# Kernel tuning notes

Hardware: AMD Instinct MI355X
Metric: run time of the kernel (lower is better)

## Reference

```python
import jax, jax.numpy as jnp
import numpy as np
from jax.ops import segment_sum, segment_max, segment_min

N_NODES = 200000
N_HE = 100000     # number of hyperedges (nets)
NNZ = 1000000     # number of pins (node,hyperedge) incidences
F_RAW = 29        # raw node features; +2 fake_pos +1 ismacro = 32 = num_features
PIN_D = 4
C = 64            # nhid (heads = 1)
N_MACRO = 512
NUM_CLASSES = 1
SLOPE = 0.1


def _lrelu(v):
    return jnp.where(v >= 0, v, SLOPE * v)


def setup_inputs() -> dict:
    key = jax.random.key(0)
    ks = jax.random.split(key, 16)
    x = jax.random.normal(ks[0], (N_NODES, F_RAW), jnp.float32)
    fake_pos = jax.random.uniform(ks[1], (N_NODES, 2), dtype=jnp.float32)
    node_idx = jax.random.randint(ks[2], (NNZ,), 0, N_NODES)
    he_idx = jax.random.randint(ks[3], (NNZ,), 0, N_HE)
    edge_index = jnp.stack([node_idx, he_idx]).astype(jnp.int32)
    pin_feature = jax.random.normal(ks[4], (NNZ, PIN_D), jnp.float32)
    macro_index = jax.random.randint(ks[5], (N_MACRO,), 0, N_NODES).astype(jnp.int32)
    F_IN = F_RAW + 3

    def lin(k, fi, fo):
        return (jax.random.normal(k, (fi, fo), jnp.float32) / np.float32(np.sqrt(fi)))

    W1 = lin(ks[6], F_IN, C); b1 = jnp.zeros((C,), jnp.float32)
    Wpin = lin(ks[7], PIN_D, C)
    att = jax.random.normal(ks[8], (2 * C,), jnp.float32) / np.float32(np.sqrt(2 * C))
    Wpost = lin(ks[9], 4 * C, C); bpost = jnp.zeros((C,), jnp.float32)
    Wm1 = lin(ks[10], 2 * C, C); bm1 = jnp.zeros((C,), jnp.float32)
    Wm2 = lin(ks[11], C, C // 2); bm2 = jnp.zeros((C // 2,), jnp.float32)
    Wm3 = lin(ks[12], C // 2, NUM_CLASSES); bm3 = jnp.zeros((NUM_CLASSES,), jnp.float32)
    return dict(x=x, fake_pos=fake_pos, edge_index=edge_index, pin_feature=pin_feature,
                macro_index=macro_index, W1=W1, b1=b1, Wpin=Wpin, att=att,
                Wpost=Wpost, bpost=bpost, Wm1=Wm1, bm1=bm1, Wm2=Wm2, bm2=bm2,
                Wm3=Wm3, bm3=bm3)


def _forward(x, fake_pos, edge_index, pin_feature, macro_index,
             W1, b1, Wpin, att, Wpost, bpost, Wm1, bm1, Wm2, bm2, Wm3, bm3):
    node_idx = edge_index[0]
    he_idx = edge_index[1]

    ismacro = jnp.zeros((N_NODES, 1), x.dtype).at[macro_index].set(1.0)
    h = jnp.concatenate([x, fake_pos, ismacro], axis=-1)  # (N, 32)

    xl = h @ W1 + b1                                      # (N, C) node embedding
    pin_m = pin_feature @ Wpin                            # (NNZ, C) pin embedding

    # node -> hyperedge aggregation (mean over incident pins)
    msg_ne = xl[node_idx] + pin_m                         # (NNZ, C)
    deg_e = segment_sum(jnp.ones((NNZ,), x.dtype), he_idx, num_segments=N_HE)
    e_feat = segment_sum(msg_ne, he_idx, num_segments=N_HE) / jnp.maximum(deg_e, 1.0)[:, None]

    # attention over incident hyperedges, softmax per node
    e_g = e_feat[he_idx]                                  # (NNZ, C)
    a_raw = _lrelu(jnp.concatenate([xl[node_idx], e_g], axis=-1) @ att)  # (NNZ,)
    m = segment_max(a_raw, node_idx, num_segments=N_NODES)
    m = jnp.where(jnp.isfinite(m), m, 0.0)
    ex = jnp.exp(a_raw - m[node_idx])
    den = segment_sum(ex, node_idx, num_segments=N_NODES)
    alpha = ex / (den[node_idx] + 1e-16)

    # hyperedge -> node: PNA multi-aggregation of attention-weighted messages
    msg = e_g * alpha[:, None]                            # (NNZ, C)
    deg_n = segment_sum(jnp.ones((NNZ,), x.dtype), node_idx, num_segments=N_NODES)
    deg_c = jnp.maximum(deg_n, 1.0)[:, None]
    s = segment_sum(msg, node_idx, num_segments=N_NODES)
    mean = s / deg_c
    mx = segment_max(msg, node_idx, num_segments=N_NODES)
    mx = jnp.where(deg_n[:, None] > 0, mx, 0.0)
    mn = segment_min(msg, node_idx, num_segments=N_NODES)
    mn = jnp.where(deg_n[:, None] > 0, mn, 0.0)
    sq = segment_sum(msg * msg, node_idx, num_segments=N_NODES) / deg_c
    std = jnp.sqrt(jnp.maximum(sq - mean * mean, 0.0) + 1e-12)

    pna = jnp.concatenate([mean, mx, mn, std], axis=-1) @ Wpost + bpost  # (N, C)
    hx = _lrelu(pna)

    # masked global-mean pools (single graph: batch is all zeros)
    pooled = jnp.concatenate([hx[macro_index].mean(0), hx.mean(0)])[None, :]  # (1, 2C)

    z = _lrelu(pooled @ Wm1 + bm1)
    z = _lrelu(z @ Wm2 + bm2)
    return z @ Wm3 + bm3                                  # (1, num_classes)


def reference(x, fake_pos, edge_index, pin_feature, macro_index,
              W1, b1, Wpin, att, Wpost, bpost, Wm1, bm1, Wm2, bm2, Wm3, bm3):
    return _forward(x, fake_pos, edge_index, pin_feature, macro_index,
                    W1, b1, Wpin, att, Wpost, bpost, Wm1, bm1, Wm2, bm2, Wm3, bm3)
```

## Files before the change

### kernel.cpp

```cpp
#include <hip/hip_runtime.h>
#include <math.h>

#define N_NODES 200000
#define N_HE    100000
#define NNZ     1000000
#define F_RAW   29
#define N_MACRO 512
#define SLOPE   0.1f
#define L_TOTAL (N_NODES + N_HE)
#define NB_SCAN 293

typedef __attribute__((ext_vector_type(8))) short bf16x8;
typedef __attribute__((ext_vector_type(4))) float f32x4;

__device__ __forceinline__ float lrelu(float v) { return v >= 0.f ? v : SLOPE * v; }
__device__ __forceinline__ float bf2f(unsigned short u) { return __uint_as_float(((unsigned)u) << 16); }
__device__ __forceinline__ unsigned short f2bf(float f) {
    unsigned u = __float_as_uint(f);
    unsigned r = u + 0x7FFFu + ((u >> 16) & 1u);
    return (unsigned short)(r >> 16);
}
__device__ __forceinline__ float bflo(unsigned u) { return __uint_as_float(u << 16); }
__device__ __forceinline__ float bfhi(unsigned u) { return __uint_as_float(u & 0xffff0000u); }

__global__ __launch_bounds__(256) void fill_f32(float* p, long long n, float v) {
    long long i = (long long)blockIdx.x * blockDim.x + threadIdx.x;
    long long st = (long long)gridDim.x * blockDim.x;
    for (; i < n; i += st) p[i] = v;
}

__global__ __launch_bounds__(256) void k_pre(
    const int* __restrict__ mi, float* __restrict__ ismacro, int* __restrict__ mcount,
    const float* __restrict__ W1, const float* __restrict__ b1,
    const float* __restrict__ att, float* __restrict__ va,
    const int* __restrict__ nidx, const int* __restrict__ hidx,
    int* __restrict__ cnt, int* __restrict__ rank_n, int* __restrict__ rank_e)
{
    if (blockIdx.x == 0) {
        int t = threadIdx.x;
        if (t < 32) {
            float a = 0.f;
            for (int c = 0; c < 64; c++) a += W1[t * 64 + c] * att[c];
            va[t] = a;
        } else if (t == 32) {
            float a = 0.f;
            for (int c = 0; c < 64; c++) a += b1[c] * att[c];
            va[32] = a;
        }
    } else if (blockIdx.x <= 2) {
        int i = (blockIdx.x - 1) * 256 + threadIdx.x;
        if (i < N_MACRO) {
            ismacro[mi[i]] = 1.0f;
            atomicAdd(&mcount[mi[i]], 1);
        }
    } else {
        int i = (blockIdx.x - 3) * 256 + threadIdx.x;
        int st = (gridDim.x - 3) * 256;
        for (int p = i; p < NNZ; p += st) {
            rank_n[p] = atomicAdd(&cnt[nidx[p]], 1);
            rank_e[p] = atomicAdd(&cnt[N_NODES + hidx[p]], 1);
        }
    }
}

__global__ __launch_bounds__(256) void k_scan1(const int* __restrict__ cnt,
                                               int* __restrict__ row_ptr, int* __restrict__ partials)
{
    __shared__ int sA[256], sB[256];
    const int t = threadIdx.x;
    const int base = blockIdx.x * 1024 + t * 4;
    int v0 = base + 0 < L_TOTAL ? cnt[base + 0] : 0;
    int v1 = base + 1 < L_TOTAL ? cnt[base + 1] : 0;
    int v2 = base + 2 < L_TOTAL ? cnt[base + 2] : 0;
    int v3 = base + 3 < L_TOTAL ? cnt[base + 3] : 0;
    sA[t] = v0 + v1 + v2 + v3;
    __syncthreads();
    int* src = sA; int* dst = sB;
    for (int off = 1; off < 256; off <<= 1) {
        int v = src[t];
        if (t >= off) v += src[t - off];
        dst[t] = v;
        __syncthreads();
        int* tmp = src; src = dst; dst = tmp;
    }
    int excl = t > 0 ? src[t - 1] : 0;
    if (base + 0 < L_TOTAL) row_ptr[base + 0] = excl;
    if (base + 1 < L_TOTAL) row_ptr[base + 1] = excl + v0;
    if (base + 2 < L_TOTAL) row_ptr[base + 2] = excl + v0 + v1;
    if (base + 3 < L_TOTAL) row_ptr[base + 3] = excl + v0 + v1 + v2;
    if (t == 255) partials[blockIdx.x] = src[255];
}

__global__ __launch_bounds__(512) void k_scan2(int* __restrict__ partials)
{
    __shared__ int sA[512], sB[512];
    const int t = threadIdx.x;
    sA[t] = t < NB_SCAN ? partials[t] : 0;
    __syncthreads();
    int* src = sA; int* dst = sB;
    for (int off = 1; off < 512; off <<= 1) {
        int v = src[t];
        if (t >= off) v += src[t - off];
        dst[t] = v;
        __syncthreads();
        int* tmp = src; src = dst; dst = tmp;
    }
    if (t < NB_SCAN) partials[t] = t > 0 ? src[t - 1] : 0;
    if (t == 0) partials[NB_SCAN] = src[511];
}

__global__ __launch_bounds__(256) void k_scan3(int* __restrict__ row_ptr, const int* __restrict__ partials)
{
    const int base = blockIdx.x * 1024 + threadIdx.x * 4;
    int add = partials[blockIdx.x];
    #pragma unroll
    for (int k = 0; k < 4; k++)
        if (base + k < L_TOTAL) row_ptr[base + k] += add;
    if (blockIdx.x == 0 && threadIdx.x == 0) row_ptr[L_TOTAL] = partials[NB_SCAN];
}

__global__ __launch_bounds__(256) void k_mid(
    const int* __restrict__ nidx, const int* __restrict__ hidx,
    const int* __restrict__ row_ptr,
    const int* __restrict__ rank_n, const int* __restrict__ rank_e,
    const float4* __restrict__ pf4, int* __restrict__ csr_n, int4* __restrict__ rec,
    const float* __restrict__ x, const float* __restrict__ fp,
    const float* __restrict__ ismacro, const float* __restrict__ va,
    unsigned short* __restrict__ h, float* __restrict__ xn_att)
{
    if (blockIdx.x < 2048) {
        int i = blockIdx.x * 256 + threadIdx.x;
        int st = 2048 * 256;
        for (int p = i; p < NNZ; p += st) {
            int n = nidx[p], e = hidx[p];
            csr_n[row_ptr[n] + rank_n[p]] = e;
            int pe = row_ptr[N_NODES + e] + rank_e[p];
            float4 q = pf4[p];
            int4 r;
            r.x = n;
            r.y = (int)((unsigned)f2bf(q.x) | ((unsigned)f2bf(q.y) << 16));
            r.z = (int)((unsigned)f2bf(q.z) | ((unsigned)f2bf(q.w) << 16));
            r.w = 0;
            rec[pe - NNZ] = r;
        }
    } else {
        const int lane = threadIdx.x & 63;
        const int half = lane >> 5, k = lane & 31;
        int wid = ((blockIdx.x - 2048) * 256 + threadIdx.x) >> 6;
        int nw = (1024 * 256) >> 6;
        float vak = va[k];
        float c0 = va[32];
        for (int base = wid * 2; base < N_NODES; base += nw * 2) {
            int n = base + half;
            float v;
            if (k < 29)       v = x[(size_t)n * F_RAW + k];
            else if (k == 29) v = fp[2 * n];
            else if (k == 30) v = fp[2 * n + 1];
            else              v = ismacro[n];
            h[(size_t)n * 32 + k] = f2bf(v);
            float r = v * vak;
            #pragma unroll
            for (int o = 16; o > 0; o >>= 1) r += __shfl_xor(r, o, 32);
            if (k == 0) xn_att[n] = r + c0;
        }
    }
}

__global__ __launch_bounds__(256) void k_he_agg(
    const int* __restrict__ row_ptr, const int4* __restrict__ rec,
    const float* __restrict__ W1, const float* __restrict__ Wpin,
    const float* __restrict__ b1, const float* __restrict__ att,
    const unsigned short* __restrict__ h,
    unsigned short* __restrict__ e_feat, float* __restrict__ e_att)
{
    __shared__ float sW1[32 * 64];
    __shared__ float sWp[4 * 64];
    __shared__ float sb1[64];
    for (int i = threadIdx.x; i < 32 * 64; i += 256) sW1[i] = W1[i];
    for (int i = threadIdx.x; i < 4 * 64; i += 256) sWp[i] = Wpin[i];
    if (threadIdx.x < 64) sb1[threadIdx.x] = b1[threadIdx.x];
    __syncthreads();
    const int lane = threadIdx.x & 63;
    const int g  = lane >> 3;
    const int gl = lane & 7;
    float att2 = att[64 + lane];
    int wid = (blockIdx.x * blockDim.x + threadIdx.x) >> 6;
    int nw = (gridDim.x * blockDim.x) >> 6;
    for (int e = wid; e < N_HE; e += nw) {
        int start = row_ptr[N_NODES + e];
        int deg = row_ptr[N_NODES + e + 1] - start;
        float h0 = 0.f, h1 = 0.f, h2 = 0.f, h3 = 0.f;
        float pa = 0.f, pb = 0.f;
        const int4* rbase = rec + (start - NNZ);
        int t = g;
        for (; t + 8 < deg; t += 16) {
            int4 rA = rbase[t];
            int4 rB = rbase[t + 8];
            ushort4 uA = *(const ushort4*)&h[(size_t)rA.x * 32 + 4 * gl];
            ushort4 uB = *(const ushort4*)&h[(size_t)rB.x * 32 + 4 * gl];
            h0 += bf2f(uA.x) + bf2f(uB.x);
            h1 += bf2f(uA.y) + bf2f(uB.y);
            h2 += bf2f(uA.z) + bf2f(uB.z);
            h3 += bf2f(uA.w) + bf2f(uB.w);
            unsigned pyA = (gl == 0) ? (unsigned)rA.y : ((gl == 1) ? (unsigned)rA.z : 0u);
            unsigned pyB = (gl == 0) ? (unsigned)rB.y : ((gl == 1) ? (unsigned)rB.z : 0u);
            pa += bflo(pyA) + bflo(pyB);
            pb += bfhi(pyA) + bfhi(pyB);
        }
        if (t < deg) {
            int4 r = rbase[t];
            ushort4 u = *(const ushort4*)&h[(size_t)r.x * 32 + 4 * gl];
            h0 += bf2f(u.x); h1 += bf2f(u.y); h2 += bf2f(u.z); h3 += bf2f(u.w);
            unsigned py = (gl == 0) ? (unsigned)r.y : ((gl == 1) ? (unsigned)r.z : 0u);
            pa += bflo(py); pb += bfhi(py);
        }
        #pragma unroll
        for (int o = 8; o <= 32; o <<= 1) {
            h0 += __shfl_xor(h0, o); h1 += __shfl_xor(h1, o);
            h2 += __shfl_xor(h2, o); h3 += __shfl_xor(h3, o);
            pa += __shfl_xor(pa, o); pb += __shfl_xor(pb, o);
        }
        float p0 = __shfl(pa, 0, 64), p1 = __shfl(pb, 0, 64);
        float p2 = __shfl(pa, 1, 64), p3 = __shfl(pb, 1, 64);
        float acc = (float)deg * sb1[lane]
                  + p0 * sWp[lane] + p1 * sWp[64 + lane]
                  + p2 * sWp[128 + lane] + p3 * sWp[192 + lane];
        #pragma unroll
        for (int kk = 0; kk < 8; kk++) {
            float a0 = __shfl(h0, kk, 64), a1 = __shfl(h1, kk, 64);
            float a2 = __shfl(h2, kk, 64), a3 = __shfl(h3, kk, 64);
            acc += a0 * sW1[(4 * kk + 0) * 64 + lane] + a1 * sW1[(4 * kk + 1) * 64 + lane]
                 + a2 * sW1[(4 * kk + 2) * 64 + lane] + a3 * sW1[(4 * kk + 3) * 64 + lane];
        }
        float d = (float)(deg > 0 ? deg : 1);
        float v = acc / d;
        e_feat[(size_t)e * 64 + lane] = f2bf(v);
        float r = v * att2;
        #pragma unroll
        for (int o = 32; o > 0; o >>= 1) r += __shfl_down(r, o, 64);
        if (lane == 0) e_att[e] = r;
    }
}

__global__ __launch_bounds__(256, 4) void k_fused(
    const int* __restrict__ row_ptr, const int* __restrict__ csr,
    const float* __restrict__ xn_att, const float* __restrict__ e_att,
    const unsigned short* __restrict__ e_feat,
    const float* __restrict__ Wpost, const float* __restrict__ bpost,
    const int* __restrict__ mcount,
    float* __restrict__ sum_all, float* __restrict__ sum_mac)
{
    __shared__ __align__(16) unsigned short scat[16 * 264];
    const int lane = threadIdx.x & 63;
    const int wave = threadIdx.x >> 6;
    const int half = lane >> 5;
    const int c2   = lane & 31;
    const int quad = lane >> 4;
    const int nn   = lane & 15;
    bf16x8 wfrag[8];
    #pragma unroll
    for (int s = 0; s < 8; s++) {
        bf16x8 w;
        #pragma unroll
        for (int j = 0; j < 8; j++)
            w[j] = (short)f2bf(Wpost[(size_t)(32 * s + quad * 8 + j) * 64 + wave * 16 + nn]);
        wfrag[s] = w;
    }
    float bias = bpost[wave * 16 + nn];
    float pool = 0.f, pmac = 0.f;
    const int nbatches = N_NODES / 16;
    for (int b = blockIdx.x; b < nbatches; b += gridDim.x) {
        const int base = b * 16;
        __syncthreads();
        for (int i = 0; i < 4; i++) {
            int j = wave * 4 + i;
            int n = base + j;
            int start = row_ptr[n];
            int deg = row_ptr[n + 1] - start;
            float xn = xn_att[n];
            float sw = 0.f;
            float sx = 0.f, sy = 0.f, qx = 0.f, qy = 0.f;
            float mxx = -INFINITY, mxy = -INFINITY, mnx = INFINITY, mny = INFINITY;
            int t = half;
            for (; t + 2 < deg; t += 4) {
                int e0 = csr[start + t];
                int e1 = csr[start + t + 2];
                float w0 = __expf(lrelu(xn + e_att[e0]));
                float w1 = __expf(lrelu(xn + e_att[e1]));
                unsigned u0 = ((const unsigned*)&e_feat[(size_t)e0 * 64])[c2];
                unsigned u1 = ((const unsigned*)&e_feat[(size_t)e1 * 64])[c2];
                float v0x = bflo(u0) * w0, v0y = bfhi(u0) * w0;
                float v1x = bflo(u1) * w1, v1y = bfhi(u1) * w1;
                sw += w0 + w1;
                sx += v0x + v1x; sy += v0y + v1y;
                qx += v0x * v0x + v1x * v1x; qy += v0y * v0y + v1y * v1y;
                mxx = fmaxf(mxx, fmaxf(v0x, v1x)); mxy = fmaxf(mxy, fmaxf(v0y, v1y));
                mnx = fminf(mnx, fminf(v0x, v1x)); mny = fminf(mny, fminf(v0y, v1y));
            }
            for (; t < deg; t += 2) {
                int e = csr[start + t];
                float w = __expf(lrelu(xn + e_att[e]));
                unsigned u = ((const unsigned*)&e_feat[(size_t)e * 64])[c2];
                float vx = bflo(u) * w, vy = bfhi(u) * w;
                sw += w; sx += vx; sy += vy; qx += vx * vx; qy += vy * vy;
                mxx = fmaxf(mxx, vx); mxy = fmaxf(mxy, vy);
                mnx = fminf(mnx, vx); mny = fminf(mny, vy);
            }
            sw  += __shfl_xor(sw, 32);
            sx  += __shfl_xor(sx, 32);  sy += __shfl_xor(sy, 32);
            qx  += __shfl_xor(qx, 32);  qy += __shfl_xor(qy, 32);
            mxx = fmaxf(mxx, __shfl_xor(mxx, 32)); mxy = fmaxf(mxy, __shfl_xor(mxy, 32));
            mnx = fminf(mnx, __shfl_xor(mnx, 32)); mny = fminf(mny, __shfl_xor(mny, 32));
            float invD = 1.f / (sw + 1e-16f);
            float dc = (float)(deg > 0 ? deg : 1);
            float meanx = sx * invD / dc, meany = sy * invD / dc;
            float sqmx = qx * invD * invD / dc, sqmy = qy * invD * invD / dc;
            float stdx = sqrtf(fmaxf(sqmx - meanx * meanx, 0.f) + 1e-12f);
            float stdy = sqrtf(fmaxf(sqmy - meany * meany, 0.f) + 1e-12f);
            ushort2* row = (ushort2*)&scat[j * 264];
            if (half == 0) {
                ushort2 a; a.x = f2bf(meanx); a.y = f2bf(meany);
                row[c2] = a;
                ushort2 bmax; bmax.x = f2bf(deg > 0 ? mxx * invD : 0.f);
                bmax.y = f2bf(deg > 0 ? mxy * invD : 0.f);
                row[32 + c2] = bmax;
            } else {
                ushort2 bmin; bmin.x = f2bf(deg > 0 ? mnx * invD : 0.f);
                bmin.y = f2bf(deg > 0 ? mny * invD : 0.f);
                row[64 + c2] = bmin;
                ushort2 bstd; bstd.x = f2bf(stdx); bstd.y = f2bf(stdy);
                row[96 + c2] = bstd;
            }
        }
        __syncthreads();
        f32x4 acc = {0.f, 0.f, 0.f, 0.f};
        #pragma unroll
        for (int s = 0; s < 8; s++) {
            bf16x8 a = *(const bf16x8*)&scat[nn * 264 + 32 * s + quad * 8];
            acc = __builtin_amdgcn_mfma_f32_16x16x32_bf16(a, wfrag[s], acc, 0, 0, 0);
        }
        int4 mc4 = *(const int4*)&mcount[base + 4 * quad];
        float h0 = lrelu(acc[0] + bias);
        float h1 = lrelu(acc[1] + bias);
        float h2 = lrelu(acc[2] + bias);
        float h3 = lrelu(acc[3] + bias);
        pool += h0 + h1 + h2 + h3;
        pmac += (float)mc4.x * h0 + (float)mc4.y * h1 + (float)mc4.z * h2 + (float)mc4.w * h3;
    }
    pool += __shfl_xor(pool, 16); pool += __shfl_xor(pool, 32);
    pmac += __shfl_xor(pmac, 16); pmac += __shfl_xor(pmac, 32);
    if (quad == 0) {
        atomicAdd(&sum_all[wave * 16 + nn], pool);
        atomicAdd(&sum_mac[wave * 16 + nn], pmac);
    }
}

__global__ __launch_bounds__(256) void k_final(
    const float* __restrict__ sum_all, const float* __restrict__ sum_mac,
    const float* __restrict__ Wm1, const float* __restrict__ bm1,
    const float* __restrict__ Wm2, const float* __restrict__ bm2,
    const float* __restrict__ Wm3, const float* __restrict__ bm3,
    float* __restrict__ out)
{
    __shared__ float spool[128];
    __shared__ float z1[64];
    __shared__ float z2[32];
    if (threadIdx.x < 64) {
        spool[threadIdx.x]      = sum_mac[threadIdx.x] / (float)N_MACRO;
        spool[64 + threadIdx.x] = sum_all[threadIdx.x] / (float)N_NODES;
    }
    __syncthreads();
    if (threadIdx.x < 64) {
        int j = threadIdx.x;
        float a = bm1[j];
        #pragma unroll 4
        for (int k = 0; k < 128; k++) a += spool[k] * Wm1[k * 64 + j];
        z1[j] = lrelu(a);
    }
    __syncthreads();
    if (threadIdx.x < 32) {
        int j = threadIdx.x;
        float a = bm2[j];
        #pragma unroll 4
        for (int k = 0; k < 64; k++) a += z1[k] * Wm2[k * 32 + j];
        z2[j] = lrelu(a);
    }
    __syncthreads();
    if (threadIdx.x == 0) {
        float a = bm3[0];
        #pragma unroll
        for (int k = 0; k < 32; k++) a += z2[k] * Wm3[k];
        out[0] = a;
    }
}

extern "C" void kernel_launch(void* const* d_in, const int* in_sizes, int n_in,
                              void* d_out, int out_size, void* d_ws, size_t ws_size,
                              hipStream_t stream)
{
    const float* x        = (const float*)d_in[0];
    const float* fake_pos = (const float*)d_in[1];
    const int*   edge     = (const int*)d_in[2];
    const float* pinf     = (const float*)d_in[3];
    const int*   macro    = (const int*)d_in[4];
    const float* W1    = (const float*)d_in[5];
    const float* b1    = (const float*)d_in[6];
    const float* Wpin  = (const float*)d_in[7];
    const float* att   = (const float*)d_in[8];
    const float* Wpost = (const float*)d_in[9];
    const float* bpost = (const float*)d_in[10];
    const float* Wm1   = (const float*)d_in[11];
    const float* bm1   = (const float*)d_in[12];
    const float* Wm2   = (const float*)d_in[13];
    const float* bm2   = (const float*)d_in[14];
    const float* Wm3   = (const float*)d_in[15];
    const float* bm3   = (const float*)d_in[16];
    float* out = (float*)d_out;

    float* ws = (float*)d_ws;
    float*    ismacro = ws;
    float*    sum_all = ws + 200000;
    float*    sum_mac = ws + 200064;
    int*      mcount  = (int*)(ws + 200128);
    int*      cnt     = (int*)(ws + 400128);
    int*      row_ptr  = (int*)(ws + 700128);
    int*      partials = (int*)(ws + 1000132);
    float*    va       = ws + 1000432;
    int*      rank_n   = (int*)(ws + 1000472);
    int*      rank_e   = (int*)(ws + 2000472);
    int*      csr_n    = (int*)(ws + 3000472);
    int4*     rec      = (int4*)(ws + 4000472);
    float*    e_att    = ws + 8000472;
    float*    xn_att   = ws + 8100472;
    unsigned short* h      = (unsigned short*)(ws + 8300472);
    unsigned short* e_feat = (unsigned short*)(ws + 11500472);

    const int* nidx = edge;
    const int* hidx = edge + NNZ;

    fill_f32<<<1024, 256, 0, stream>>>(ws, 700128LL, 0.f);
    k_pre<<<2051, 256, 0, stream>>>(macro, ismacro, mcount, W1, b1, att, va,
                                    nidx, hidx, cnt, rank_n, rank_e);
    k_scan1<<<NB_SCAN, 256, 0, stream>>>(cnt, row_ptr, partials);
    k_scan2<<<1, 512, 0, stream>>>(partials);
    k_scan3<<<NB_SCAN, 256, 0, stream>>>(row_ptr, partials);
    k_mid<<<3072, 256, 0, stream>>>(nidx, hidx, row_ptr, rank_n, rank_e,
                                    (const float4*)pinf, csr_n, rec,
                                    x, fake_pos, ismacro, va, h, xn_att);
    k_he_agg<<<2048, 256, 0, stream>>>(row_ptr, rec, W1, Wpin, b1, att, h, e_feat, e_att);
    k_fused<<<2048, 256, 0, stream>>>(row_ptr, csr_n, xn_att, e_att, e_feat, Wpost, bpost,
                                      mcount, sum_all, sum_mac);
    k_final<<<1, 256, 0, stream>>>(sum_all, sum_mac, Wm1, bm1, Wm2, bm2, Wm3, bm3, out);
}
```

Before: 474.0 us.

## Make node aggregation wave-independent and precompute transposed bf16 Wpost

Each wave in the fused node kernel now owns a 16-node batch, builds its own shared-memory tile, and computes all 64 output channels by reading a pre-transposed bf16 Wpost from global memory. This removes the block-wide barriers and the per-block Wpost conversion. The node-feature/attention work also moves into the counting kernel so it overlaps with the atomic counting, and the pin scatter becomes a separate kernel. In exchange, Wpost is re-read from cache on every batch, each wave needs 4x the shared memory, and there is one more kernel launch.

```diff
diff --git a/kernel.cpp b/kernel.cpp
--- a/kernel.cpp
+++ b/kernel.cpp
@@ -29,12 +29,11 @@
     for (; i < n; i += st) p[i] = v;
 }
 
-__global__ __launch_bounds__(256) void k_pre(
+__global__ __launch_bounds__(256) void k_tiny(
     const int* __restrict__ mi, float* __restrict__ ismacro, int* __restrict__ mcount,
     const float* __restrict__ W1, const float* __restrict__ b1,
     const float* __restrict__ att, float* __restrict__ va,
-    const int* __restrict__ nidx, const int* __restrict__ hidx,
-    int* __restrict__ cnt, int* __restrict__ rank_n, int* __restrict__ rank_e)
+    const float* __restrict__ Wpost, unsigned short* __restrict__ Wt)
 {
     if (blockIdx.x == 0) {
         int t = threadIdx.x;
@@ -55,75 +54,16 @@
         }
     } else {
         int i = (blockIdx.x - 3) * 256 + threadIdx.x;
-        int st = (gridDim.x - 3) * 256;
-        for (int p = i; p < NNZ; p += st) {
-            rank_n[p] = atomicAdd(&cnt[nidx[p]], 1);
-            rank_e[p] = atomicAdd(&cnt[N_NODES + hidx[p]], 1);
-        }
-    }
-}
-
-__global__ __launch_bounds__(256) void k_scan1(const int* __restrict__ cnt,
-                                               int* __restrict__ row_ptr, int* __restrict__ partials)
-{
-    __shared__ int sA[256], sB[256];
-    const int t = threadIdx.x;
-    const int base = blockIdx.x * 1024 + t * 4;
-    int v0 = base + 0 < L_TOTAL ? cnt[base + 0] : 0;
-    int v1 = base + 1 < L_TOTAL ? cnt[base + 1] : 0;
-    int v2 = base + 2 < L_TOTAL ? cnt[base + 2] : 0;
-    int v3 = base + 3 < L_TOTAL ? cnt[base + 3] : 0;
-    sA[t] = v0 + v1 + v2 + v3;
-    __syncthreads();
-    int* src = sA; int* dst = sB;
-    for (int off = 1; off < 256; off <<= 1) {
-        int v = src[t];
-        if (t >= off) v += src[t - off];
-        dst[t] = v;
-        __syncthreads();
-        int* tmp = src; src = dst; dst = tmp;
-    }
-    int excl = t > 0 ? src[t - 1] : 0;
-    if (base + 0 < L_TOTAL) row_ptr[base + 0] = excl;
-    if (base + 1 < L_TOTAL) row_ptr[base + 1] = excl + v0;
-    if (base + 2 < L_TOTAL) row_ptr[base + 2] = excl + v0 + v1;
-    if (base + 3 < L_TOTAL) row_ptr[base + 3] = excl + v0 + v1 + v2;
-    if (t == 255) partials[blockIdx.x] = src[255];
-}
-
-__global__ __launch_bounds__(512) void k_scan2(int* __restrict__ partials)
-{
-    __shared__ int sA[512], sB[512];
-    const int t = threadIdx.x;
-    sA[t] = t < NB_SCAN ? partials[t] : 0;
-    __syncthreads();
-    int* src = sA; int* dst = sB;
-    for (int off = 1; off < 512; off <<= 1) {
-        int v = src[t];
-        if (t >= off) v += src[t - off];
-        dst[t] = v;
-        __syncthreads();
-        int* tmp = src; src = dst; dst = tmp;
-    }
-    if (t < NB_SCAN) partials[t] = t > 0 ? src[t - 1] : 0;
-    if (t == 0) partials[NB_SCAN] = src[511];
-}
-
-__global__ __launch_bounds__(256) void k_scan3(int* __restrict__ row_ptr, const int* __restrict__ partials)
-{
-    const int base = blockIdx.x * 1024 + threadIdx.x * 4;
-    int add = partials[blockIdx.x];
-    #pragma unroll
-    for (int k = 0; k < 4; k++)
-        if (base + k < L_TOTAL) row_ptr[base + k] += add;
-    if (blockIdx.x == 0 && threadIdx.x == 0) row_ptr[L_TOTAL] = partials[NB_SCAN];
-}
-
-__global__ __launch_bounds__(256) void k_mid(
+        for (int e = i; e < 64 * 256; e += 8 * 256) {
+            int c = e >> 8, k = e & 255;
+            Wt[c * 256 + k] = f2bf(Wpost[k * 64 + c]);
+        }
+    }
+}
+
+__global__ __launch_bounds__(256) void k_cnt_h(
     const int* __restrict__ nidx, const int* __restrict__ hidx,
-    const int* __restrict__ row_ptr,
-    const int* __restrict__ rank_n, const int* __restrict__ rank_e,
-    const float4* __restrict__ pf4, int* __restrict__ csr_n, int4* __restrict__ rec,
+    int* __restrict__ cnt, int* __restrict__ rank_n, int* __restrict__ rank_e,
     const float* __restrict__ x, const float* __restrict__ fp,
     const float* __restrict__ ismacro, const float* __restrict__ va,
     unsigned short* __restrict__ h, float* __restrict__ xn_att)
@@ -132,16 +72,8 @@
         int i = blockIdx.x * 256 + threadIdx.x;
         int st = 2048 * 256;
         for (int p = i; p < NNZ; p += st) {
-            int n = nidx[p], e = hidx[p];
-            csr_n[row_ptr[n] + rank_n[p]] = e;
-            int pe = row_ptr[N_NODES + e] + rank_e[p];
-            float4 q = pf4[p];
-            int4 r;
-            r.x = n;
-            r.y = (int)((unsigned)f2bf(q.x) | ((unsigned)f2bf(q.y) << 16));
-            r.z = (int)((unsigned)f2bf(q.z) | ((unsigned)f2bf(q.w) << 16));
-            r.w = 0;
-            rec[pe - NNZ] = r;
+            rank_n[p] = atomicAdd(&cnt[nidx[p]], 1);
+            rank_e[p] = atomicAdd(&cnt[N_NODES + hidx[p]], 1);
         }
     } else {
         const int lane = threadIdx.x & 63;
@@ -163,6 +95,84 @@
             for (int o = 16; o > 0; o >>= 1) r += __shfl_xor(r, o, 32);
             if (k == 0) xn_att[n] = r + c0;
         }
+    }
+}
+
+__global__ __launch_bounds__(256) void k_scan1(const int* __restrict__ cnt,
+                                               int* __restrict__ row_ptr, int* __restrict__ partials)
+{
+    __shared__ int sA[256], sB[256];
+    const int t = threadIdx.x;
+    const int base = blockIdx.x * 1024 + t * 4;
+    int v0 = base + 0 < L_TOTAL ? cnt[base + 0] : 0;
+    int v1 = base + 1 < L_TOTAL ? cnt[base + 1] : 0;
+    int v2 = base + 2 < L_TOTAL ? cnt[base + 2] : 0;
+    int v3 = base + 3 < L_TOTAL ? cnt[base + 3] : 0;
+    sA[t] = v0 + v1 + v2 + v3;
+    __syncthreads();
+    int* src = sA; int* dst = sB;
+    for (int off = 1; off < 256; off <<= 1) {
+        int v = src[t];
+        if (t >= off) v += src[t - off];
+        dst[t] = v;
+        __syncthreads();
+        int* tmp = src; src = dst; dst = tmp;
+    }
+    int excl = t > 0 ? src[t - 1] : 0;
+    if (base + 0 < L_TOTAL) row_ptr[base + 0] = excl;
+    if (base + 1 < L_TOTAL) row_ptr[base + 1] = excl + v0;
+    if (base + 2 < L_TOTAL) row_ptr[base + 2] = excl + v0 + v1;
+    if (base + 3 < L_TOTAL) row_ptr[base + 3] = excl + v0 + v1 + v2;
+    if (t == 255) partials[blockIdx.x] = src[255];
+}
+
+__global__ __launch_bounds__(512) void k_scan2(int* __restrict__ partials)
+{
+    __shared__ int sA[512], sB[512];
+    const int t = threadIdx.x;
+    sA[t] = t < NB_SCAN ? partials[t] : 0;
+    __syncthreads();
+    int* src = sA; int* dst = sB;
+    for (int off = 1; off < 512; off <<= 1) {
+        int v = src[t];
+        if (t >= off) v += src[t - off];
+        dst[t] = v;
+        __syncthreads();
+        int* tmp = src; src = dst; dst = tmp;
+    }
+    if (t < NB_SCAN) partials[t] = t > 0 ? src[t - 1] : 0;
+    if (t == 0) partials[NB_SCAN] = src[511];
+}
+
+__global__ __launch_bounds__(256) void k_scan3(int* __restrict__ row_ptr, const int* __restrict__ partials)
+{
+    const int base = blockIdx.x * 1024 + threadIdx.x * 4;
+    int add = partials[blockIdx.x];
+    #pragma unroll
+    for (int k = 0; k < 4; k++)
+        if (base + k < L_TOTAL) row_ptr[base + k] += add;
+    if (blockIdx.x == 0 && threadIdx.x == 0) row_ptr[L_TOTAL] = partials[NB_SCAN];
+}
+
+__global__ __launch_bounds__(256) void k_scatter(
+    const int* __restrict__ nidx, const int* __restrict__ hidx,
+    const int* __restrict__ row_ptr,
+    const int* __restrict__ rank_n, const int* __restrict__ rank_e,
+    const float4* __restrict__ pf4, int* __restrict__ csr_n, int4* __restrict__ rec)
+{
+    int i = blockIdx.x * 256 + threadIdx.x;
+    int st = gridDim.x * 256;
+    for (int p = i; p < NNZ; p += st) {
+        int n = nidx[p], e = hidx[p];
+        csr_n[row_ptr[n] + rank_n[p]] = e;
+        int pe = row_ptr[N_NODES + e] + rank_e[p];
+        float4 q = pf4[p];
+        int4 r;
+        r.x = n;
+        r.y = (int)((unsigned)f2bf(q.x) | ((unsigned)f2bf(q.y) << 16));
+        r.z = (int)((unsigned)f2bf(q.z) | ((unsigned)f2bf(q.w) << 16));
+        r.w = 0;
+        rec[pe - NNZ] = r;
     }
 }
 
@@ -246,34 +256,28 @@
     const int* __restrict__ row_ptr, const int* __restrict__ csr,
     const float* __restrict__ xn_att, const float* __restrict__ e_att,
     const unsigned short* __restrict__ e_feat,
-    const float* __restrict__ Wpost, const float* __restrict__ bpost,
+    const unsigned short* __restrict__ Wt, const float* __restrict__ bpost,
     const int* __restrict__ mcount,
     float* __restrict__ sum_all, float* __restrict__ sum_mac)
 {
-    __shared__ __align__(16) unsigned short scat[16 * 264];
+    __shared__ __align__(16) unsigned short scat[4][16 * 264];
     const int lane = threadIdx.x & 63;
     const int wave = threadIdx.x >> 6;
     const int half = lane >> 5;
     const int c2   = lane & 31;
     const int quad = lane >> 4;
     const int nn   = lane & 15;
-    bf16x8 wfrag[8];
-    #pragma unroll
-    for (int s = 0; s < 8; s++) {
-        bf16x8 w;
-        #pragma unroll
-        for (int j = 0; j < 8; j++)
-            w[j] = (short)f2bf(Wpost[(size_t)(32 * s + quad * 8 + j) * 64 + wave * 16 + nn]);
-        wfrag[s] = w;
-    }
-    float bias = bpost[wave * 16 + nn];
-    float pool = 0.f, pmac = 0.f;
+    unsigned short* ws = &scat[wave][0];
+    float bias0 = bpost[0 * 16 + nn], bias1 = bpost[1 * 16 + nn];
+    float bias2 = bpost[2 * 16 + nn], bias3 = bpost[3 * 16 + nn];
+    float pool0 = 0.f, pool1 = 0.f, pool2 = 0.f, pool3 = 0.f;
+    float pmac0 = 0.f, pmac1 = 0.f, pmac2 = 0.f, pmac3 = 0.f;
     const int nbatches = N_NODES / 16;
-    for (int b = blockIdx.x; b < nbatches; b += gridDim.x) {
+    const int wid0 = blockIdx.x * 4 + wave;
+    const int nwv = gridDim.x * 4;
+    for (int b = wid0; b < nbatches; b += nwv) {
         const int base = b * 16;
-        __syncthreads();
-        for (int i = 0; i < 4; i++) {
-            int j = wave * 4 + i;
+        for (int j = 0; j < 16; j++) {
             int n = base + j;
             int start = row_ptr[n];
             int deg = row_ptr[n + 1] - start;
@@ -317,7 +321,7 @@
             float sqmx = qx * invD * invD / dc, sqmy = qy * invD * invD / dc;
             float stdx = sqrtf(fmaxf(sqmx - meanx * meanx, 0.f) + 1e-12f);
             float stdy = sqrtf(fmaxf(sqmy - meany * meany, 0.f) + 1e-12f);
-            ushort2* row = (ushort2*)&scat[j * 264];
+            ushort2* row = (ushort2*)&ws[j * 264];
             if (half == 0) {
                 ushort2 a; a.x = f2bf(meanx); a.y = f2bf(meany);
                 row[c2] = a;
@@ -332,26 +336,40 @@
                 row[96 + c2] = bstd;
             }
         }
-        __syncthreads();
-        f32x4 acc = {0.f, 0.f, 0.f, 0.f};
+        int4 mc4 = *(const int4*)&mcount[base + 4 * quad];
         #pragma unroll
-        for (int s = 0; s < 8; s++) {
-            bf16x8 a = *(const bf16x8*)&scat[nn * 264 + 32 * s + quad * 8];
-            acc = __builtin_amdgcn_mfma_f32_16x16x32_bf16(a, wfrag[s], acc, 0, 0, 0);
-        }
-        int4 mc4 = *(const int4*)&mcount[base + 4 * quad];
-        float h0 = lrelu(acc[0] + bias);
-        float h1 = lrelu(acc[1] + bias);
-        float h2 = lrelu(acc[2] + bias);
-        float h3 = lrelu(acc[3] + bias);
-        pool += h0 + h1 + h2 + h3;
-        pmac += (float)mc4.x * h0 + (float)mc4.y * h1 + (float)mc4.z * h2 + (float)mc4.w * h3;
-    }
-    pool += __shfl_xor(pool, 16); pool += __shfl_xor(pool, 32);
-    pmac += __shfl_xor(pmac, 16); pmac += __shfl_xor(pmac, 32);
-    if (quad == 0) {
-        atomicAdd(&sum_all[wave * 16 + nn], pool);
-        atomicAdd(&sum_mac[wave * 16 + nn], pmac);
+        for (int r = 0; r < 4; r++) {
+            f32x4 acc = {0.f, 0.f, 0.f, 0.f};
+            #pragma unroll
+            for (int s = 0; s < 8; s++) {
+                bf16x8 a = *(const bf16x8*)&ws[nn * 264 + 32 * s + quad * 8];
+                bf16x8 bw = *(const bf16x8*)&Wt[(size_t)(r * 16 + nn) * 256 + 32 * s + quad * 8];
+                acc = __builtin_amdgcn_mfma_f32_16x16x32_bf16(a, bw, acc, 0, 0, 0);
+            }
+            float bias = r == 0 ? bias0 : (r == 1 ? bias1 : (r == 2 ? bias2 : bias3));
+            float h0 = lrelu(acc[0] + bias);
+            float h1 = lrelu(acc[1] + bias);
+            float h2 = lrelu(acc[2] + bias);
+            float h3 = lrelu(acc[3] + bias);
+            float ps = h0 + h1 + h2 + h3;
+            float pm = (float)mc4.x * h0 + (float)mc4.y * h1
+                     + (float)mc4.z * h2 + (float)mc4.w * h3;
+            if (r == 0) { pool0 += ps; pmac0 += pm; }
+            else if (r == 1) { pool1 += ps; pmac1 += pm; }
+            else if (r == 2) { pool2 += ps; pmac2 += pm; }
+            else { pool3 += ps; pmac3 += pm; }
+        }
+    }
+    #pragma unroll
+    for (int r = 0; r < 4; r++) {
+        float ps = r == 0 ? pool0 : (r == 1 ? pool1 : (r == 2 ? pool2 : pool3));
+        float pm = r == 0 ? pmac0 : (r == 1 ? pmac1 : (r == 2 ? pmac2 : pmac3));
+        ps += __shfl_xor(ps, 16); ps += __shfl_xor(ps, 32);
+        pm += __shfl_xor(pm, 16); pm += __shfl_xor(pm, 32);
+        if (quad == 0) {
+            atomicAdd(&sum_all[r * 16 + nn], ps);
+            atomicAdd(&sum_mac[r * 16 + nn], pm);
+        }
     }
 }
 
@@ -426,29 +444,30 @@
     int*      row_ptr  = (int*)(ws + 700128);
     int*      partials = (int*)(ws + 1000132);
     float*    va       = ws + 1000432;
-    int*      rank_n   = (int*)(ws + 1000472);
-    int*      rank_e   = (int*)(ws + 2000472);
-    int*      csr_n    = (int*)(ws + 3000472);
-    int4*     rec      = (int4*)(ws + 4000472);
-    float*    e_att    = ws + 8000472;
-    float*    xn_att   = ws + 8100472;
-    unsigned short* h      = (unsigned short*)(ws + 8300472);
-    unsigned short* e_feat = (unsigned short*)(ws + 11500472);
+    unsigned short* Wt = (unsigned short*)(ws + 1000472);
+    int*      rank_n   = (int*)(ws + 1008664);
+    int*      rank_e   = (int*)(ws + 2008664);
+    int*      csr_n    = (int*)(ws + 3008664);
+    int4*     rec      = (int4*)(ws + 4008664);
+    float*    e_att    = ws + 8008664;
+    float*    xn_att   = ws + 8108664;
+    unsigned short* h      = (unsigned short*)(ws + 8308664);
+    unsigned short* e_feat = (unsigned short*)(ws + 11508664);
 
     const int* nidx = edge;
     const int* hidx = edge + NNZ;
 
     fill_f32<<<1024, 256, 0, stream>>>(ws, 700128LL, 0.f);
-    k_pre<<<2051, 256, 0, stream>>>(macro, ismacro, mcount, W1, b1, att, va,
-                                    nidx, hidx, cnt, rank_n, rank_e);
+    k_tiny<<<11, 256, 0, stream>>>(macro, ismacro, mcount, W1, b1, att, va, Wpost, Wt);
+    k_cnt_h<<<3072, 256, 0, stream>>>(nidx, hidx, cnt, rank_n, rank_e,
+                                      x, fake_pos, ismacro, va, h, xn_att);
     k_scan1<<<NB_SCAN, 256, 0, stream>>>(cnt, row_ptr, partials);
     k_scan2<<<1, 512, 0, stream>>>(partials);
     k_scan3<<<NB_SCAN, 256, 0, stream>>>(row_ptr, partials);
-    k_mid<<<3072, 256, 0, stream>>>(nidx, hidx, row_ptr, rank_n, rank_e,
-                                    (const float4*)pinf, csr_n, rec,
-                                    x, fake_pos, ismacro, va, h, xn_att);
+    k_scatter<<<2048, 256, 0, stream>>>(nidx, hidx, row_ptr, rank_n, rank_e,
+                                        (const float4*)pinf, csr_n, rec);
     k_he_agg<<<2048, 256, 0, stream>>>(row_ptr, rec, W1, Wpin, b1, att, h, e_feat, e_att);
-    k_fused<<<2048, 256, 0, stream>>>(row_ptr, csr_n, xn_att, e_att, e_feat, Wpost, bpost,
+    k_fused<<<2048, 256, 0, stream>>>(row_ptr, csr_n, xn_att, e_att, e_feat, Wt, bpost,
                                       mcount, sum_all, sum_mac);
     k_final<<<1, 256, 0, stream>>>(sum_all, sum_mac, Wm1, bm1, Wm2, bm2, Wm3, bm3, out);
 }
```

Result: slower. 677.1 us (+42.9%).
